# Kernel tuning notes

Measured on AMD Instinct MI355X. Metric: run time of the kernel, lower is better.

## Reference

```python
import jax, jax.numpy as jnp
import numpy as np

E = 320000   # edges
N = 10000    # nodes (len(set(idx_i)))
F = 128      # feature dim f
NRBF = 20    # n
R_CUT = 5.0


def setup_inputs() -> dict:
    key = jax.random.key(0)
    ks = jax.random.split(key, 8)
    s = jax.random.normal(ks[0], (E, 1, F), dtype=jnp.float32)
    r = jax.random.normal(ks[1], (E, 3), dtype=jnp.float32)
    v = jax.random.normal(ks[2], (E, 3, F), dtype=jnp.float32)
    idx_i = jax.random.randint(ks[3], (E,), 0, N)
    # phi layer: Linear(F -> 3F), internal_w_layer: Linear(NRBF -> 3F)
    W_phi = jax.random.normal(ks[4], (F, 3 * F), dtype=jnp.float32) * 0.02
    b_phi = jnp.zeros((3 * F,), dtype=jnp.float32)
    W_w = jax.random.normal(ks[5], (NRBF, 3 * F), dtype=jnp.float32) * 0.02
    b_w = jnp.zeros((3 * F,), dtype=jnp.float32)
    return {"s": s, "r": r, "v": v, "idx_i": idx_i,
            "W_phi": W_phi, "b_phi": b_phi, "W_w": W_w, "b_w": b_w}


def reference(s, r, v, idx_i, W_phi, b_phi, W_w, b_w):
    # phi(s): [E,1,3F]
    phi_out = s @ W_phi + b_phi
    org_r = jax.lax.stop_gradient(r)            # r.detach().clone()
    # RBF: sin(n*pi/r_cut * |r|) / |r|  -> [E,1,NRBF]
    r_norm = jnp.linalg.norm(r, axis=1, keepdims=True)[..., None]   # [E,1,1]
    n_vals = jnp.arange(1, NRBF + 1, dtype=s.dtype)                 # [NRBF]
    rbf = jnp.sin(n_vals * (jnp.pi / R_CUT) * r_norm) / r_norm      # [E,1,NRBF]
    # cosine cutoff applied to rbf values (faithful to the source)
    rbf = jnp.where(rbf <= R_CUT, 0.5 * (jnp.cos(jnp.pi * rbf / R_CUT) + 1.0), 0.0)
    w = rbf @ W_w + b_w                          # [E,1,3F]
    split = w * phi_out                          # [E,1,3F]
    sv, ss, sr = split[..., :F], split[..., F:2 * F], split[..., 2 * F:]
    # scalar messages: scatter-add ss into nodes -> [N,1,F]
    out_s = jax.ops.segment_sum(ss, idx_i, num_segments=N)
    # vector messages
    org_rn = org_r / jnp.linalg.norm(org_r)      # global Frobenius norm (faithful)
    vr = sr * org_rn[:, :, None]                 # [E,3,F]
    v_msg = sv * v + vr                          # [E,3,F]
    out_v = jax.ops.segment_sum(v_msg, idx_i, num_segments=N)  # [N,3,F]
    return (out_v, out_s)
```

## Files before the change

kernel.cpp:

```cpp
#include <hip/hip_runtime.h>

#define E_EDGES 320000
#define N_NODES 10000
#define F_DIM   128
#define C_DIM   384
#define NRBF_K  20
#define TILE    16
#define TP      20
#define PI_F    3.14159265358979323846f

__global__ void sumsq_kernel(const float* __restrict__ r,
                             float* __restrict__ out) {
    __shared__ float red[4];
    int tid = blockIdx.x * blockDim.x + threadIdx.x;
    int stride = gridDim.x * blockDim.x;
    float acc = 0.f;
    for (int i = tid; i < E_EDGES * 3; i += stride) {
        float x = r[i];
        acc += x * x;
    }
    #pragma unroll
    for (int off = 32; off > 0; off >>= 1)
        acc += __shfl_down(acc, off, 64);
    int lane = threadIdx.x & 63;
    int wave = threadIdx.x >> 6;
    if (lane == 0) red[wave] = acc;
    __syncthreads();
    if (threadIdx.x == 0) {
        float s = red[0] + red[1] + red[2] + red[3];
        atomicAdd(out, s);
    }
}

__global__ __launch_bounds__(384) void main_kernel(
    const float* __restrict__ s,
    const float* __restrict__ r,
    const float* __restrict__ v,
    const int*   __restrict__ idx_i,
    const float* __restrict__ W_phi,
    const float* __restrict__ b_phi,
    const float* __restrict__ W_w,
    const float* __restrict__ b_w,
    const float* __restrict__ sumsq,
    float* __restrict__ out_v,
    float* __restrict__ out_s)
{
    __shared__ float s_tile[F_DIM][TP];
    __shared__ float rbf_sh[NRBF_K][TP];
    __shared__ float orn_sh[TILE][3];
    __shared__ float split_sh[C_DIM][TILE + 1];
    __shared__ int   idx_sh[TILE];

    const int tid = threadIdx.x;
    const int j   = tid;
    const float inv_gn = rsqrtf(*sumsq);
    const float bp = b_phi[j];
    const float bw = b_w[j];

    const int ntiles = E_EDGES / TILE;
    for (int t = blockIdx.x; t < ntiles; t += gridDim.x) {
        const int e0 = t * TILE;

        for (int q = tid; q < TILE * F_DIM; q += 384) {
            int e = q >> 7, k = q & 127;
            s_tile[k][e] = s[(size_t)(e0 + e) * F_DIM + k];
        }
        if (tid < TILE * NRBF_K) {
            int e = tid / NRBF_K, n = tid % NRBF_K;
            float r0 = r[(e0 + e) * 3 + 0];
            float r1 = r[(e0 + e) * 3 + 1];
            float r2 = r[(e0 + e) * 3 + 2];
            float rn = sqrtf(r0 * r0 + r1 * r1 + r2 * r2);
            float arg  = (float)(n + 1) * (PI_F / 5.0f) * rn;
            float tval = sinf(arg) / rn;
            float env  = (tval <= 5.0f) ? 0.5f * (cosf(PI_F * tval / 5.0f) + 1.0f)
                                        : 0.0f;
            rbf_sh[n][e] = env;
        }
        if (tid >= 320 && tid < 320 + TILE * 3) {
            int q = tid - 320; int e = q / 3, d = q % 3;
            orn_sh[e][d] = r[(e0 + e) * 3 + d] * inv_gn;
        }
        if (tid >= 368) {
            idx_sh[tid - 368] = idx_i[e0 + (tid - 368)];
        }
        __syncthreads();

        float accp[TILE], accw[TILE];
        #pragma unroll
        for (int e = 0; e < TILE; e++) { accp[e] = bp; accw[e] = bw; }

        for (int k = 0; k < F_DIM; k++) {
            float wv = W_phi[k * C_DIM + j];
            const float4* s4 = (const float4*)(&s_tile[k][0]);
            float sv[TILE];
            *(float4*)&sv[0]  = s4[0];
            *(float4*)&sv[4]  = s4[1];
            *(float4*)&sv[8]  = s4[2];
            *(float4*)&sv[12] = s4[3];
            #pragma unroll
            for (int e = 0; e < TILE; e++) accp[e] += wv * sv[e];
        }
        #pragma unroll
        for (int n = 0; n < NRBF_K; n++) {
            float wv = W_w[n * C_DIM + j];
            const float4* r4 = (const float4*)(&rbf_sh[n][0]);
            float rv[TILE];
            *(float4*)&rv[0]  = r4[0];
            *(float4*)&rv[4]  = r4[1];
            *(float4*)&rv[8]  = r4[2];
            *(float4*)&rv[12] = r4[3];
            #pragma unroll
            for (int e = 0; e < TILE; e++) accw[e] += wv * rv[e];
        }
        #pragma unroll
        for (int e = 0; e < TILE; e++) split_sh[j][e] = accp[e] * accw[e];
        __syncthreads();

        const int f = tid & 127;
        const int d = tid >> 7;
        for (int e = 0; e < TILE; e++) {
            int   idx = idx_sh[e];
            float svv = split_sh[f][e];
            float srr = split_sh[256 + f][e];
            float vv  = v[(size_t)(e0 + e) * C_DIM + tid];
            float msg = svv * vv + srr * orn_sh[e][d];
            atomicAdd(&out_v[((size_t)idx * 3 + d) * F_DIM + f], msg);
            if (d == 0) {
                float ss = split_sh[128 + f][e];
                atomicAdd(&out_s[(size_t)idx * F_DIM + f], ss);
            }
        }
        __syncthreads();
    }
}

extern "C" void kernel_launch(void* const* d_in, const int* in_sizes, int n_in,
                              void* d_out, int out_size, void* d_ws, size_t ws_size,
                              hipStream_t stream) {
    const float* s     = (const float*)d_in[0];
    const float* r     = (const float*)d_in[1];
    const float* v     = (const float*)d_in[2];
    const int*   idx_i = (const int*)d_in[3];
    const float* W_phi = (const float*)d_in[4];
    const float* b_phi = (const float*)d_in[5];
    const float* W_w   = (const float*)d_in[6];
    const float* b_w   = (const float*)d_in[7];

    float* out   = (float*)d_out;
    float* sumsq = (float*)d_ws;
    const int NV = N_NODES * 3 * F_DIM;

    hipMemsetAsync(d_out, 0, (size_t)out_size * sizeof(float), stream);
    hipMemsetAsync(d_ws, 0, 16, stream);
    sumsq_kernel<<<512, 256, 0, stream>>>(r, sumsq);
    main_kernel<<<1024, 384, 0, stream>>>(s, r, v, idx_i, W_phi, b_phi, W_w, b_w,
                                          sumsq, out, out + NV);
}
```

Before: 2.099 ms.

## Register-tile edges per wave and drop shared split buffer in edge kernel

Restructures the main kernel to 256 threads where each wave owns 8 edges of a 32-edge tile and each lane computes two columns in each of the three channel groups, keeping phi and w accumulators in registers. The split values are multiplied and scattered directly from registers, removing the shared split buffer and one barrier per tile, and v loads become float2. This raises per-thread register pressure (96 accumulators) and changes the atomic access pattern to paired adjacent addresses. Grid size and launch bounds are adjusted to match.

```diff
diff --git a/kernel.cpp b/kernel.cpp
--- a/kernel.cpp
+++ b/kernel.cpp
@@ -5,8 +5,8 @@
 #define F_DIM   128
 #define C_DIM   384
 #define NRBF_K  20
-#define TILE    16
-#define TP      20
+#define TILE    32
+#define TP      36
 #define PI_F    3.14159265358979323846f
 
 __global__ void sumsq_kernel(const float* __restrict__ r,
@@ -32,7 +32,7 @@
     }
 }
 
-__global__ __launch_bounds__(384) void main_kernel(
+__global__ __launch_bounds__(256, 3) void main_kernel(
     const float* __restrict__ s,
     const float* __restrict__ r,
     const float* __restrict__ v,
@@ -48,88 +48,120 @@
     __shared__ float s_tile[F_DIM][TP];
     __shared__ float rbf_sh[NRBF_K][TP];
     __shared__ float orn_sh[TILE][3];
-    __shared__ float split_sh[C_DIM][TILE + 1];
     __shared__ int   idx_sh[TILE];
 
     const int tid = threadIdx.x;
-    const int j   = tid;
+    const int cl  = tid & 63;
+    const int wv  = tid >> 6;
+    const int e8  = wv * 8;
     const float inv_gn = rsqrtf(*sumsq);
-    const float bp = b_phi[j];
-    const float bw = b_w[j];
+
+    const float2* Wp2 = (const float2*)W_phi;
+    const float2* Ww2 = (const float2*)W_w;
+    const float2 bp0 = ((const float2*)b_phi)[cl];
+    const float2 bp1 = ((const float2*)b_phi)[cl + 64];
+    const float2 bp2 = ((const float2*)b_phi)[cl + 128];
+    const float2 bw0 = ((const float2*)b_w)[cl];
+    const float2 bw1 = ((const float2*)b_w)[cl + 64];
+    const float2 bw2 = ((const float2*)b_w)[cl + 128];
 
     const int ntiles = E_EDGES / TILE;
     for (int t = blockIdx.x; t < ntiles; t += gridDim.x) {
         const int e0 = t * TILE;
 
-        for (int q = tid; q < TILE * F_DIM; q += 384) {
-            int e = q >> 7, k = q & 127;
-            s_tile[k][e] = s[(size_t)(e0 + e) * F_DIM + k];
+        {
+            const int k  = tid & 127;
+            const int eb = tid >> 7;
+            #pragma unroll
+            for (int i = 0; i < 16; i++) {
+                int e = eb + 2 * i;
+                s_tile[k][e] = s[(size_t)(e0 + e) * F_DIM + k];
+            }
         }
-        if (tid < TILE * NRBF_K) {
-            int e = tid / NRBF_K, n = tid % NRBF_K;
+        for (int q = tid; q < TILE * NRBF_K; q += 256) {
+            int e = q / NRBF_K;
+            int n = q - e * NRBF_K;
             float r0 = r[(e0 + e) * 3 + 0];
             float r1 = r[(e0 + e) * 3 + 1];
             float r2 = r[(e0 + e) * 3 + 2];
             float rn = sqrtf(r0 * r0 + r1 * r1 + r2 * r2);
             float arg  = (float)(n + 1) * (PI_F / 5.0f) * rn;
-            float tval = sinf(arg) / rn;
-            float env  = (tval <= 5.0f) ? 0.5f * (cosf(PI_F * tval / 5.0f) + 1.0f)
+            float tv   = sinf(arg) / rn;
+            rbf_sh[n][e] = (tv <= 5.0f) ? 0.5f * (cosf(PI_F * tv / 5.0f) + 1.0f)
                                         : 0.0f;
-            rbf_sh[n][e] = env;
         }
-        if (tid >= 320 && tid < 320 + TILE * 3) {
-            int q = tid - 320; int e = q / 3, d = q % 3;
-            orn_sh[e][d] = r[(e0 + e) * 3 + d] * inv_gn;
-        }
-        if (tid >= 368) {
-            idx_sh[tid - 368] = idx_i[e0 + (tid - 368)];
+        if (tid < TILE) {
+            float r0 = r[(e0 + tid) * 3 + 0];
+            float r1 = r[(e0 + tid) * 3 + 1];
+            float r2 = r[(e0 + tid) * 3 + 2];
+            orn_sh[tid][0] = r0 * inv_gn;
+            orn_sh[tid][1] = r1 * inv_gn;
+            orn_sh[tid][2] = r2 * inv_gn;
+            idx_sh[tid] = idx_i[e0 + tid];
         }
         __syncthreads();
 
-        float accp[TILE], accw[TILE];
+        float2 ap0[8], ap1[8], ap2[8];
+        float2 aw0[8], aw1[8], aw2[8];
         #pragma unroll
-        for (int e = 0; e < TILE; e++) { accp[e] = bp; accw[e] = bw; }
+        for (int e = 0; e < 8; e++) {
+            ap0[e] = bp0; ap1[e] = bp1; ap2[e] = bp2;
+            aw0[e] = bw0; aw1[e] = bw1; aw2[e] = bw2;
+        }
+
+        #pragma unroll
+        for (int n = 0; n < NRBF_K; n++) {
+            float2 w0 = Ww2[n * 192 + cl];
+            float2 w1 = Ww2[n * 192 + 64 + cl];
+            float2 w2 = Ww2[n * 192 + 128 + cl];
+            float sv[8];
+            *(float4*)&sv[0] = *(const float4*)&rbf_sh[n][e8];
+            *(float4*)&sv[4] = *(const float4*)&rbf_sh[n][e8 + 4];
+            #pragma unroll
+            for (int e = 0; e < 8; e++) {
+                aw0[e].x += w0.x * sv[e]; aw0[e].y += w0.y * sv[e];
+                aw1[e].x += w1.x * sv[e]; aw1[e].y += w1.y * sv[e];
+                aw2[e].x += w2.x * sv[e]; aw2[e].y += w2.y * sv[e];
+            }
+        }
 
         for (int k = 0; k < F_DIM; k++) {
-            float wv = W_phi[k * C_DIM + j];
-            const float4* s4 = (const float4*)(&s_tile[k][0]);
-            float sv[TILE];
-            *(float4*)&sv[0]  = s4[0];
-            *(float4*)&sv[4]  = s4[1];
-            *(float4*)&sv[8]  = s4[2];
-            *(float4*)&sv[12] = s4[3];
+            float2 w0 = Wp2[k * 192 + cl];
+            float2 w1 = Wp2[k * 192 + 64 + cl];
+            float2 w2 = Wp2[k * 192 + 128 + cl];
+            float sv[8];
+            *(float4*)&sv[0] = *(const float4*)&s_tile[k][e8];
+            *(float4*)&sv[4] = *(const float4*)&s_tile[k][e8 + 4];
             #pragma unroll
-            for (int e = 0; e < TILE; e++) accp[e] += wv * sv[e];
+            for (int e = 0; e < 8; e++) {
+                ap0[e].x += w0.x * sv[e]; ap0[e].y += w0.y * sv[e];
+                ap1[e].x += w1.x * sv[e]; ap1[e].y += w1.y * sv[e];
+                ap2[e].x += w2.x * sv[e]; ap2[e].y += w2.y * sv[e];
+            }
         }
+
         #pragma unroll
-        for (int n = 0; n < NRBF_K; n++) {
-            float wv = W_w[n * C_DIM + j];
-            const float4* r4 = (const float4*)(&rbf_sh[n][0]);
-            float rv[TILE];
-            *(float4*)&rv[0]  = r4[0];
-            *(float4*)&rv[4]  = r4[1];
-            *(float4*)&rv[8]  = r4[2];
-            *(float4*)&rv[12] = r4[3];
-            #pragma unroll
-            for (int e = 0; e < TILE; e++) accw[e] += wv * rv[e];
-        }
-        #pragma unroll
-        for (int e = 0; e < TILE; e++) split_sh[j][e] = accp[e] * accw[e];
-        __syncthreads();
-
-        const int f = tid & 127;
-        const int d = tid >> 7;
-        for (int e = 0; e < TILE; e++) {
-            int   idx = idx_sh[e];
-            float svv = split_sh[f][e];
-            float srr = split_sh[256 + f][e];
-            float vv  = v[(size_t)(e0 + e) * C_DIM + tid];
-            float msg = svv * vv + srr * orn_sh[e][d];
-            atomicAdd(&out_v[((size_t)idx * 3 + d) * F_DIM + f], msg);
-            if (d == 0) {
-                float ss = split_sh[128 + f][e];
-                atomicAdd(&out_s[(size_t)idx * F_DIM + f], ss);
-            }
+        for (int e = 0; e < 8; e++) {
+            const int ee  = e8 + e;
+            const int idx = idx_sh[ee];
+            const size_t vb = (size_t)(e0 + ee) * C_DIM + 2 * cl;
+            float2 v0 = *(const float2*)&v[vb];
+            float2 v1 = *(const float2*)&v[vb + 128];
+            float2 v2 = *(const float2*)&v[vb + 256];
+            float o0 = orn_sh[ee][0], o1 = orn_sh[ee][1], o2 = orn_sh[ee][2];
+            float svx = ap0[e].x * aw0[e].x, svy = ap0[e].y * aw0[e].y;
+            float ssx = ap1[e].x * aw1[e].x, ssy = ap1[e].y * aw1[e].y;
+            float srx = ap2[e].x * aw2[e].x, sry = ap2[e].y * aw2[e].y;
+            float* ovp = out_v + (size_t)idx * C_DIM + 2 * cl;
+            atomicAdd(ovp,       svx * v0.x + srx * o0);
+            atomicAdd(ovp + 1,   svy * v0.y + sry * o0);
+            atomicAdd(ovp + 128, svx * v1.x + srx * o1);
+            atomicAdd(ovp + 129, svy * v1.y + sry * o1);
+            atomicAdd(ovp + 256, svx * v2.x + srx * o2);
+            atomicAdd(ovp + 257, svy * v2.y + sry * o2);
+            float* osp = out_s + (size_t)idx * F_DIM + 2 * cl;
+            atomicAdd(osp,     ssx);
+            atomicAdd(osp + 1, ssy);
         }
         __syncthreads();
     }
@@ -154,6 +186,6 @@
     hipMemsetAsync(d_out, 0, (size_t)out_size * sizeof(float), stream);
     hipMemsetAsync(d_ws, 0, 16, stream);
     sumsq_kernel<<<512, 256, 0, stream>>>(r, sumsq);
-    main_kernel<<<1024, 384, 0, stream>>>(s, r, v, idx_i, W_phi, b_phi, W_w, b_w,
+    main_kernel<<<2048, 256, 0, stream>>>(s, r, v, idx_i, W_phi, b_phi, W_w, b_w,
                                           sumsq, out, out + NV);
 }
```

Measured after the change: 2.769 ms. 31.9% more time.
